# Optimization experiments

Hardware: AMD Instinct MI355X
Metric: run time of the kernel (lower is better)

The kernel has to match this reference:

```python
import jax, jax.numpy as jnp
import numpy as np

B, T, C, HS = 4, 2048, 2048, 64
H = C // HS
LW, LA, LV, LG = 64, 64, 32, 128
EPS_GN = 0.00064


def setup_inputs() -> dict:
    key = jax.random.key(0)
    ks = jax.random.split(key, 32)
    rn = lambda k, shape, s=1.0: jax.random.normal(k, shape, dtype=jnp.float32) * s
    return {
        "x": rn(ks[0], (B, T, C)),
        "v_first": rn(ks[1], (B, T, C)),
        "x_prev": rn(ks[2], (B, C)),
        "wkv_state": rn(ks[3], (B, H, HS, HS), 0.1),
        "x_r": rn(ks[4], (C,), 0.1),
        "x_w": rn(ks[5], (C,), 0.1),
        "x_k": rn(ks[6], (C,), 0.1),
        "x_v": rn(ks[7], (C,), 0.1),
        "x_a": rn(ks[8], (C,), 0.1),
        "x_g": rn(ks[9], (C,), 0.1),
        "w0": rn(ks[10], (C,), 0.1),
        "w1": rn(ks[11], (C, LW), 0.02),
        "w2": rn(ks[12], (LW, C), 0.02),
        "a0": rn(ks[13], (C,), 0.1),
        "a1": rn(ks[14], (C, LA), 0.02),
        "a2": rn(ks[15], (LA, C), 0.02),
        "v0": rn(ks[16], (C,), 0.1),
        "v1": rn(ks[17], (C, LV), 0.02),
        "v2": rn(ks[18], (LV, C), 0.02),
        "g1": rn(ks[19], (C, LG), 0.02),
        "g2": rn(ks[20], (LG, C), 0.02),
        "k_k": rn(ks[21], (C,), 0.1),
        "k_a": rn(ks[22], (C,), 0.1),
        "r_k": rn(ks[23], (H, HS), 0.1),
        "Wr": rn(ks[24], (C, C), 0.02),
        "Wk": rn(ks[25], (C, C), 0.02),
        "Wv": rn(ks[26], (C, C), 0.02),
        "Wo": rn(ks[27], (C, C), 0.02),
        "ln_w": jnp.ones((C,), dtype=jnp.float32),
        "ln_b": jnp.zeros((C,), dtype=jnp.float32),
    }


def _fwd(x, v_first, x_prev, wkv_state, x_r, x_w, x_k, x_v, x_a, x_g,
         w0, w1, w2, a0, a1, a2, v0, v1, v2, g1, g2, k_k, k_a, r_k,
         Wr, Wk, Wv, Wo, ln_w, ln_b):
    Bb, Tt, Cc = x.shape
    # token shift
    xx = jnp.concatenate([x_prev[:, None, :], x[:, :-1, :]], axis=1) - x
    xr = x + xx * x_r; xw = x + xx * x_w; xk = x + xx * x_k
    xv = x + xx * x_v; xa = x + xx * x_a; xg = x + xx * x_g
    r = xr @ Wr
    k = xk @ Wk
    v = xv @ Wv
    # log-decay: -softplus(-(w0 + tanh(xw@w1)@w2)) - 0.5  (<= -0.5)
    w_raw = -jax.nn.softplus(-(w0 + jnp.tanh(xw @ w1) @ w2)) - 0.5
    # layer_id != 0: mix with v_first
    v = v + (v_first - v) * jax.nn.sigmoid(v0 + (xv @ v1) @ v2)
    a = jax.nn.sigmoid(a0 + (xa @ a1) @ a2)
    g = jax.nn.sigmoid(xg @ g1) @ g2
    kk = (k * k_k).reshape(Bb, Tt, H, HS)
    kk = kk / jnp.maximum(jnp.linalg.norm(kk, axis=-1, keepdims=True), 1e-12)
    k = k * (1.0 + (a - 1.0) * k_a)
    rh = r.reshape(Bb, Tt, H, HS)
    kh = k.reshape(Bb, Tt, H, HS)
    vh = v.reshape(Bb, Tt, H, HS)
    ah = -kk                                  # removal direction
    bh = kk * a.reshape(Bb, Tt, H, HS)        # insertion direction
    wd = jnp.exp(-jnp.exp(w_raw)).reshape(Bb, Tt, H, HS)  # decay in (0,1)
    def step(st, ts):
        r_t, w_t, k_t, v_t, a_t, b_t = ts     # each [B,H,N]
        sa = jnp.einsum('bhij,bhj->bhi', st, a_t)
        st = st * w_t[:, :, None, :] + sa[..., None] * b_t[:, :, None, :] \
             + v_t[..., None] * k_t[:, :, None, :]
        return st, jnp.einsum('bhij,bhj->bhi', st, r_t)
    xs = tuple(jnp.moveaxis(t, 1, 0) for t in (rh, wd, kh, vh, ah, bh))
    _, out = jax.lax.scan(step, wkv_state, xs)
    out = jnp.moveaxis(out, 0, 1)             # [B,T,H,N]
    # GroupNorm(H groups) over each head's N channels
    mu = out.mean(-1, keepdims=True)
    var = out.var(-1, keepdims=True)
    out = ((out - mu) * jax.lax.rsqrt(var + EPS_GN)).reshape(Bb, Tt, Cc) * ln_w + ln_b
    bonus = (rh * kh * r_k).sum(-1, keepdims=True) * vh
    out = out + bonus.reshape(Bb, Tt, Cc)
    return (out * g) @ Wo


def reference(x, v_first, x_prev, wkv_state, x_r, x_w, x_k, x_v, x_a, x_g,
              w0, w1, w2, a0, a1, a2, v0, v1, v2, g1, g2, k_k, k_a, r_k,
              Wr, Wk, Wv, Wo, ln_w, ln_b):
    return _fwd(x, v_first, x_prev, wkv_state, x_r, x_w, x_k, x_v, x_a, x_g,
                w0, w1, w2, a0, a1, a2, v0, v1, v2, g1, g2, k_k, k_a, r_k,
                Wr, Wk, Wv, Wo, ln_w, ln_b)
```

## Files before the change

### kernel.cpp

```cpp
#include <hip/hip_runtime.h>

typedef float f32x4 __attribute__((ext_vector_type(4)));
typedef __bf16 bf16x8 __attribute__((ext_vector_type(8)));
typedef __bf16 bf16x4 __attribute__((ext_vector_type(4)));
typedef unsigned int u32x4 __attribute__((ext_vector_type(4)));

#define DI __device__ __forceinline__

constexpr int B_ = 4, T_ = 2048, C_ = 2048, H_ = 32;
constexpr int M_ = B_ * T_;

DI unsigned short f2bf(float f) {
  unsigned u = __float_as_uint(f);
  return (unsigned short)((u + 0x7FFFu + ((u >> 16) & 1u)) >> 16);
}
DI float bf2f(unsigned short h) { return __uint_as_float(((unsigned)h) << 16); }

DI void gl16(const void* g, void* l) {
  __builtin_amdgcn_global_load_lds(
      (__attribute__((address_space(1))) const unsigned int*)g,
      (__attribute__((address_space(3))) unsigned int*)l, 16, 0, 0);
}
DI void gl4(const void* g, void* l) {
  __builtin_amdgcn_global_load_lds(
      (__attribute__((address_space(1))) const unsigned int*)g,
      (__attribute__((address_space(3))) unsigned int*)l, 4, 0, 0);
}

DI float rsum16(float x) {
  int t = __builtin_amdgcn_update_dpp(0, __float_as_int(x), 0xB1, 0xF, 0xF, true);
  x += __int_as_float(t);
  t = __builtin_amdgcn_update_dpp(0, __float_as_int(x), 0x4E, 0xF, 0xF, true);
  x += __int_as_float(t);
  t = __builtin_amdgcn_update_dpp(0, __float_as_int(x), 0x124, 0xF, 0xF, true);
  x += __int_as_float(t);
  t = __builtin_amdgcn_update_dpp(0, __float_as_int(x), 0x128, 0xF, 0xF, true);
  x += __int_as_float(t);
  return x;
}

DI void tr_body(const float* __restrict__ in, unsigned short* __restrict__ out,
                int R, int C, int bx, int by, float (*tile)[33]) {
  int c0 = bx * 32, r0 = by * 32;
  int tx = threadIdx.x & 31, ty = threadIdx.x >> 5;
#pragma unroll
  for (int i = 0; i < 4; ++i) {
    int r = r0 + ty * 4 + i, c = c0 + tx;
    if (r < R && c < C) tile[ty * 4 + i][tx] = in[(size_t)r * C + c];
  }
  __syncthreads();
#pragma unroll
  for (int i = 0; i < 4; ++i) {
    int c = c0 + ty * 4 + i, r = r0 + tx;
    if (r < R && c < C) out[(size_t)c * R + r] = f2bf(tile[tx][ty * 4 + i]);
  }
}

__global__ __launch_bounds__(256) void k_transpose(const float* __restrict__ in,
                                                   unsigned short* __restrict__ out,
                                                   int R, int C) {
  __shared__ float tile[32][33];
  tr_body(in, out, R, C, blockIdx.x, blockIdx.y, tile);
}

__global__ __launch_bounds__(256) void k_transpose8(
    const float* w1, unsigned short* W1T, const float* a1, unsigned short* A1T,
    const float* v1, unsigned short* V1T, const float* g1, unsigned short* G1T,
    const float* w2, unsigned short* W2T, const float* a2, unsigned short* A2T,
    const float* v2, unsigned short* V2T, const float* g2, unsigned short* G2T) {
  __shared__ float tile[32][33];
  int b = blockIdx.x;
  if (b < 128)       tr_body(w1, W1T, 2048, 64, b % 2, b / 2, tile);
  else if (b < 256)  { b -= 128; tr_body(a1, A1T, 2048, 64, b % 2, b / 2, tile); }
  else if (b < 320)  { b -= 256; tr_body(v1, V1T, 2048, 32, 0, b, tile); }
  else if (b < 576)  { b -= 320; tr_body(g1, G1T, 2048, 128, b % 4, b / 4, tile); }
  else if (b < 704)  { b -= 576; tr_body(w2, W2T, 64, 2048, b % 64, b / 64, tile); }
  else if (b < 832)  { b -= 704; tr_body(a2, A2T, 64, 2048, b % 64, b / 64, tile); }
  else if (b < 896)  { b -= 832; tr_body(v2, V2T, 32, 2048, b % 64, b / 64, tile); }
  else               { b -= 896; tr_body(g2, G2T, 128, 2048, b % 64, b / 64, tile); }
}

DI void mix_emit(const float* coef, int c0, size_t off,
                 const float* xv, const float* dx, unsigned short* dst) {
  unsigned short u[8];
#pragma unroll
  for (int i = 0; i < 2; ++i) {
    f32x4 cf = *(const f32x4*)(coef + c0 + i * 4);
#pragma unroll
    for (int j = 0; j < 4; ++j) u[i * 4 + j] = f2bf(xv[i * 4 + j] + dx[i * 4 + j] * cf[j]);
  }
  u32x4 pv;
#pragma unroll
  for (int j = 0; j < 4; ++j) pv[j] = (unsigned)u[2 * j] | ((unsigned)u[2 * j + 1] << 16);
  *(u32x4*)(dst + off) = pv;
}

__global__ __launch_bounds__(256) void k_prep6(
    const float* __restrict__ x, const float* __restrict__ xprev,
    const float* __restrict__ cR, const float* __restrict__ cV,
    const float* __restrict__ cK, const float* __restrict__ cW,
    const float* __restrict__ cA, const float* __restrict__ cG,
    unsigned short* __restrict__ XR, unsigned short* __restrict__ XV,
    unsigned short* __restrict__ XK, unsigned short* __restrict__ XW,
    unsigned short* __restrict__ XA, unsigned short* __restrict__ XG) {
  int bt = blockIdx.x;
  int t = bt & (T_ - 1);
  int c0 = threadIdx.x * 8;
  size_t off = (size_t)bt * C_ + c0;
  const float* xp = x + off;
  const float* pp = t ? (xp - C_) : (xprev + (size_t)(bt >> 11) * C_ + c0);
  float xv[8], dx[8];
#pragma unroll
  for (int i = 0; i < 2; ++i) {
    f32x4 a = *(const f32x4*)(xp + i * 4);
    f32x4 p = *(const f32x4*)(pp + i * 4);
#pragma unroll
    for (int j = 0; j < 4; ++j) { xv[i * 4 + j] = a[j]; dx[i * 4 + j] = p[j] - a[j]; }
  }
  mix_emit(cR, c0, off, xv, dx, XR);
  mix_emit(cV, c0, off, xv, dx, XV);
  mix_emit(cK, c0, off, xv, dx, XK);
  mix_emit(cW, c0, off, xv, dx, XW);
  mix_emit(cA, c0, off, xv, dx, XA);
  mix_emit(cG, c0, off, xv, dx, XG);
}

template <int EPI>
__global__ __launch_bounds__(256, 2) void k_gemm_big(
    const unsigned short* __restrict__ A,
    const unsigned short* __restrict__ Bt,
    float* __restrict__ outF, unsigned short* __restrict__ outB,
    const unsigned short* __restrict__ svb, const float* __restrict__ vfirst,
    const unsigned short* __restrict__ abf,
    const float* __restrict__ k_k, const float* __restrict__ k_a,
    unsigned short* __restrict__ ahb, unsigned short* __restrict__ bhb) {
  __shared__ __align__(16) unsigned short As[128][64];
  __shared__ __align__(16) unsigned short Bs[128][64];
  const int tid = threadIdx.x, lane = tid & 63, wv = tid >> 6;
  const int bid = blockIdx.x;
  const int loc = bid >> 3;
  const int by = (bid & 7) * 8 + (loc & 7);
  const int bx = loc >> 3;
  const int m0 = by * 128, n0 = bx * 128;
  const int wm = (wv >> 1) * 64, wn = (wv & 1) * 64;
  const int lr = lane >> 3, lc = (lane & 7) * 8;
  f32x4 acc[4][4] = {};
  for (int kt = 0; kt < C_; kt += 64) {
    __syncthreads();
#pragma unroll
    for (int i = 0; i < 4; ++i) {
      int chunk = wv * 4 + i, r = chunk * 8 + lr;
      gl16(A + (size_t)(m0 + r) * C_ + kt + lc, (char*)&As[0][0] + chunk * 1024);
      gl16(Bt + (size_t)(n0 + r) * C_ + kt + lc, (char*)&Bs[0][0] + chunk * 1024);
    }
    __syncthreads();
    const int rr = lane & 15;
#pragma unroll
    for (int kh = 0; kh < 2; ++kh) {
      const int kof = kh * 32 + (lane >> 4) * 8;
      bf16x8 af[4], bfv[4];
#pragma unroll
      for (int i = 0; i < 4; ++i) af[i] = *(const bf16x8*)&As[wm + i * 16 + rr][kof];
#pragma unroll
      for (int j = 0; j < 4; ++j) bfv[j] = *(const bf16x8*)&Bs[wn + j * 16 + rr][kof];
#pragma unroll
      for (int i = 0; i < 4; ++i)
#pragma unroll
        for (int j = 0; j < 4; ++j)
          acc[i][j] = __builtin_amdgcn_mfma_f32_16x16x32_bf16(af[i], bfv[j], acc[i][j], 0, 0, 0);
    }
  }
  const int cr = (lane >> 4) * 4, cc2 = lane & 15;
  if constexpr (EPI == 2) {
    float kkv[4], kav[4];
#pragma unroll
    for (int j = 0; j < 4; ++j) {
      int col = n0 + wn + j * 16 + cc2;
      kkv[j] = k_k[col];
      kav[j] = k_a[col];
    }
#pragma unroll
    for (int i = 0; i < 4; ++i)
#pragma unroll
      for (int q = 0; q < 4; ++q) {
        int row = m0 + wm + i * 16 + cr + q;
        float kk4[4], p = 0.f;
#pragma unroll
        for (int j = 0; j < 4; ++j) {
          float kkc = acc[i][j][q] * kkv[j];
          kk4[j] = kkc;
          p += kkc * kkc;
        }
        p += __shfl_xor(p, 1); p += __shfl_xor(p, 2);
        p += __shfl_xor(p, 4); p += __shfl_xor(p, 8);
        float inv = 1.f / fmaxf(sqrtf(p), 1e-12f);
#pragma unroll
        for (int j = 0; j < 4; ++j) {
          int col = n0 + wn + j * 16 + cc2;
          size_t off = (size_t)row * C_ + col;
          float kkn = kk4[j] * inv;
          float a = bf2f(abf[off]);
          ahb[off] = f2bf(-kkn);
          bhb[off] = f2bf(kkn * a);
          outB[off] = f2bf(acc[i][j][q] * (1.f + (a - 1.f) * kav[j]));
        }
      }
  } else {
#pragma unroll
    for (int i = 0; i < 4; ++i)
#pragma unroll
      for (int j = 0; j < 4; ++j)
#pragma unroll
        for (int q = 0; q < 4; ++q) {
          int row = m0 + wm + i * 16 + cr + q;
          int col = n0 + wn + j * 16 + cc2;
          size_t off = (size_t)row * C_ + col;
          float v = acc[i][j][q];
          if constexpr (EPI == 0) {
            outB[off] = f2bf(v);
          } else if constexpr (EPI == 1) {
            float s = bf2f(svb[off]);
            outB[off] = f2bf(v + (vfirst[off] - v) * s);
          } else {
            outF[off] = v;
          }
        }
  }
}

template <int N, int ACT>
DI void down_body(int m0, unsigned short (*As)[64], unsigned short (*Bs)[64],
                  const unsigned short* __restrict__ A,
                  const unsigned short* __restrict__ Bt,
                  unsigned short* __restrict__ out) {
  const int tid = threadIdx.x, lane = tid & 63, wv = tid >> 6;
  const int wm = wv * 32;
  const int lr = lane >> 3, lc = (lane & 7) * 8;
  f32x4 acc[2][N / 16] = {};
  for (int kt = 0; kt < C_; kt += 64) {
    __syncthreads();
#pragma unroll
    for (int i = 0; i < 4; ++i) {
      int chunk = wv * 4 + i, r = chunk * 8 + lr;
      gl16(A + (size_t)(m0 + r) * C_ + kt + lc, (char*)&As[0][0] + chunk * 1024);
    }
#pragma unroll
    for (int i = 0; i < N / 32; ++i) {
      int chunk = wv * (N / 32) + i, r = chunk * 8 + lr;
      gl16(Bt + (size_t)r * C_ + kt + lc, (char*)&Bs[0][0] + chunk * 1024);
    }
    __syncthreads();
    const int rr = lane & 15;
#pragma unroll
    for (int kh = 0; kh < 2; ++kh) {
      const int kof = kh * 32 + (lane >> 4) * 8;
      bf16x8 af[2], bfv[N / 16];
#pragma unroll
      for (int i = 0; i < 2; ++i) af[i] = *(const bf16x8*)&As[wm + i * 16 + rr][kof];
#pragma unroll
      for (int j = 0; j < N / 16; ++j) bfv[j] = *(const bf16x8*)&Bs[j * 16 + rr][kof];
#pragma unroll
      for (int i = 0; i < 2; ++i)
#pragma unroll
        for (int j = 0; j < N / 16; ++j)
          acc[i][j] = __builtin_amdgcn_mfma_f32_16x16x32_bf16(af[i], bfv[j], acc[i][j], 0, 0, 0);
    }
  }
  const int cr = (lane >> 4) * 4, cc2 = lane & 15;
#pragma unroll
  for (int i = 0; i < 2; ++i)
#pragma unroll
    for (int j = 0; j < N / 16; ++j)
#pragma unroll
      for (int q = 0; q < 4; ++q) {
        int row = m0 + wm + i * 16 + cr + q;
        int col = j * 16 + cc2;
        float v = acc[i][j][q];
        if (ACT == 1) v = tanhf(v);
        else if (ACT == 2) v = 1.f / (1.f + expf(-v));
        out[(size_t)row * N + col] = f2bf(v);
      }
}

__global__ __launch_bounds__(256, 2) void k_down4(
    const unsigned short* __restrict__ XMw, const unsigned short* __restrict__ XMa,
    const unsigned short* __restrict__ XMv, const unsigned short* __restrict__ XMg,
    const unsigned short* __restrict__ W1T, const unsigned short* __restrict__ A1T,
    const unsigned short* __restrict__ V1T, const unsigned short* __restrict__ G1T,
    unsigned short* __restrict__ HWB, unsigned short* __restrict__ HAB,
    unsigned short* __restrict__ HVB, unsigned short* __restrict__ HGB) {
  __shared__ __align__(16) unsigned short As[128][64];
  __shared__ __align__(16) unsigned short Bs[128][64];
  int g = blockIdx.x >> 6;
  int m0 = (blockIdx.x & 63) * 128;
  if (g == 0)      down_body<64, 1>(m0, As, Bs, XMw, W1T, HWB);
  else if (g == 1) down_body<64, 0>(m0, As, Bs, XMa, A1T, HAB);
  else if (g == 2) down_body<32, 0>(m0, As, Bs, XMv, V1T, HVB);
  else             down_body<128, 2>(m0, As, Bs, XMg, G1T, HGB);
}

template <int K, int MODE>
__global__ __launch_bounds__(256, 2) void k_up(
    const unsigned short* __restrict__ A, const unsigned short* __restrict__ Bt,
    const float* __restrict__ bias, float* __restrict__ outF,
    unsigned short* __restrict__ outB) {
  __shared__ __align__(16) unsigned short As[128][K];
  __shared__ __align__(16) unsigned short Bs[128][K];
  const int tid = threadIdx.x, lane = tid & 63, wv = tid >> 6;
  const int m0 = blockIdx.y * 128, n0 = blockIdx.x * 128;
  const int wm = (wv >> 1) * 64, wn = (wv & 1) * 64;
  constexpr int LPR = K / 8;
  constexpr int RPC = 64 / LPR;
  const int lr = lane / LPR, lc = (lane % LPR) * 8;
  f32x4 acc[4][4] = {};
#pragma unroll
  for (int i = 0; i < K / 16; ++i) {
    int chunk = wv * (K / 16) + i;
    int r = chunk * RPC + lr;
    gl16(A + (size_t)(m0 + r) * K + lc, (char*)&As[0][0] + chunk * 1024);
    gl16(Bt + (size_t)(n0 + r) * K + lc, (char*)&Bs[0][0] + chunk * 1024);
  }
  __syncthreads();
  const int rr = lane & 15;
#pragma unroll
  for (int ks = 0; ks < K / 32; ++ks) {
    const int kof = ks * 32 + (lane >> 4) * 8;
    bf16x8 af[4], bfv[4];
#pragma unroll
    for (int i = 0; i < 4; ++i) af[i] = *(const bf16x8*)&As[wm + i * 16 + rr][kof];
#pragma unroll
    for (int j = 0; j < 4; ++j) bfv[j] = *(const bf16x8*)&Bs[wn + j * 16 + rr][kof];
#pragma unroll
    for (int i = 0; i < 4; ++i)
#pragma unroll
      for (int j = 0; j < 4; ++j)
        acc[i][j] = __builtin_amdgcn_mfma_f32_16x16x32_bf16(af[i], bfv[j], acc[i][j], 0, 0, 0);
  }
  const int cr = (lane >> 4) * 4, cc2 = lane & 15;
#pragma unroll
  for (int i = 0; i < 4; ++i)
#pragma unroll
    for (int j = 0; j < 4; ++j)
#pragma unroll
      for (int q = 0; q < 4; ++q) {
        int row = m0 + wm + i * 16 + cr + q;
        int col = n0 + wn + j * 16 + cc2;
        size_t off = (size_t)row * C_ + col;
        float up = acc[i][j][q];
        if (MODE == 0) {
          float z = -(bias[col] + up);
          float sp = fmaxf(z, 0.f) + log1pf(expf(-fabsf(z)));
          outF[off] = expf(-expf(-sp - 0.5f));
        } else if (MODE == 1) {
          outB[off] = f2bf(1.f / (1.f + expf(-(bias[col] + up))));
        } else {
          outB[off] = f2bf(up);
        }
      }
}

__global__ __launch_bounds__(64, 2) void k_scan(
    const unsigned short* __restrict__ RB, const float* __restrict__ WD,
    const unsigned short* __restrict__ KB, const unsigned short* __restrict__ VB,
    const unsigned short* __restrict__ AHB, const unsigned short* __restrict__ BHB,
    const float* __restrict__ s0, float* __restrict__ out) {
  __shared__ __align__(16) char sl[8][1024];
  const int lane = threadIdx.x & 63;
  const int p = blockIdx.x;
  const int wq = p >> 7, bh = p & 127;
  const int b = bh >> 5, h = bh & 31;
  const int e = lane & 15, rl = lane >> 4;
  const int row = wq * 4 + rl;
  const size_t base = (size_t)b * T_ * C_ + h * 64;
  f32x4 S = *(const f32x4*)(s0 + ((size_t)(b * H_ + h) * 64 + row) * 64 + e * 4);

  const char* srcA = (lane < 32 ? (const char*)RB : (const char*)KB) + (lane & 31) * 4;
  const char* srcB = (lane < 32 ? (const char*)AHB : (const char*)BHB) + (lane & 31) * 4;
  const char* srcW = (const char*)WD + lane * 4;
  const char* srcV = (const char*)VB + lane * 4;

  bf16x4 rv0, kv0, av0, bv0, rv1, kv1, av1, bv1;
  f32x4 wv0, wv1;
  unsigned short vi0, vi1;

#define ISSUE(t, slot)                                                        \
  {                                                                           \
    size_t ti = (size_t)((t) < T_ ? (t) : T_ - 1);                            \
    size_t eo = base + ti * C_;                                               \
    char* d = &sl[(slot)][0];                                                 \
    gl4(srcA + 2 * eo, d);                                                    \
    gl4(srcB + 2 * eo, d + 256);                                              \
    gl4(srcW + 4 * eo, d + 512);                                              \
    gl4(srcV + 2 * eo, d + 768);                                              \
  }

#define PREF(n, slot)                                                         \
  {                                                                           \
    const char* bp = &sl[(slot)][0];                                          \
    rv##n = *(const bf16x4*)(bp + e * 8);                                     \
    kv##n = *(const bf16x4*)(bp + 128 + e * 8);                               \
    av##n = *(const bf16x4*)(bp + 256 + e * 8);                               \
    bv##n = *(const bf16x4*)(bp + 384 + e * 8);                               \
    wv##n = *(const f32x4*)(bp + 512 + e * 16);                               \
    vi##n = *(const unsigned short*)(bp + 768 + row * 2);                     \
  }

#define COMPUTE(n, t)                                                         \
  {                                                                           \
    float rr[4], kk[4], aa[4], bb[4];                                         \
    _Pragma("unroll") for (int j = 0; j < 4; ++j) {                           \
      rr[j] = (float)rv##n[j];                                                \
      kk[j] = (float)kv##n[j];                                                \
      aa[j] = (float)av##n[j];                                                \
      bb[j] = (float)bv##n[j];                                                \
    }                                                                         \
    float sa = S[0] * aa[0];                                                  \
    sa = fmaf(S[1], aa[1], sa);                                               \
    sa = fmaf(S[2], aa[2], sa);                                               \
    sa = fmaf(S[3], aa[3], sa);                                               \
    sa = rsum16(sa);                                                          \
    float vi = bf2f(vi##n);                                                   \
    float o = 0.f;                                                            \
    _Pragma("unroll") for (int j = 0; j < 4; ++j) {                           \
      S[j] = fmaf(S[j], wv##n[j], fmaf(sa, bb[j], vi * kk[j]));               \
      o = fmaf(S[j], rr[j], o);                                               \
    }                                                                         \
    o = rsum16(o);                                                            \
    if (e == 0) out[base + (size_t)(t) * C_ + row] = o;                       \
  }

#define VMW asm volatile("s_waitcnt vmcnt(12)" ::: "memory")

  ISSUE(0, 0) ISSUE(1, 1) ISSUE(2, 2) ISSUE(3, 3)
  VMW;
  PREF(0, 0)
#pragma unroll 1
  for (int t = 0; t < T_; t += 8) {
    ISSUE(t + 4, 4)  VMW; PREF(1, 1) COMPUTE(0, t + 0)
    ISSUE(t + 5, 5)  VMW; PREF(0, 2) COMPUTE(1, t + 1)
    ISSUE(t + 6, 6)  VMW; PREF(1, 3) COMPUTE(0, t + 2)
    ISSUE(t + 7, 7)  VMW; PREF(0, 4) COMPUTE(1, t + 3)
    ISSUE(t + 8, 0)  VMW; PREF(1, 5) COMPUTE(0, t + 4)
    ISSUE(t + 9, 1)  VMW; PREF(0, 6) COMPUTE(1, t + 5)
    ISSUE(t + 10, 2) VMW; PREF(1, 7) COMPUTE(0, t + 6)
    ISSUE(t + 11, 3) VMW; PREF(0, 0) COMPUTE(1, t + 7)
  }
#undef ISSUE
#undef PREF
#undef COMPUTE
#undef VMW
}

__global__ __launch_bounds__(256) void k_gn(
    const float* __restrict__ o, const unsigned short* __restrict__ rb,
    const unsigned short* __restrict__ kb, const unsigned short* __restrict__ v,
    const unsigned short* __restrict__ g, const float* __restrict__ r_k,
    const float* __restrict__ lnw, const float* __restrict__ lnb,
    unsigned short* __restrict__ outg) {
  int wid = blockIdx.x * 4 + (threadIdx.x >> 6);
  int lane = threadIdx.x & 63;
  int h = wid & (H_ - 1);
  size_t bt = (size_t)(wid >> 5);
  size_t off = bt * C_ + h * 64 + lane;
  int c = h * 64 + lane;
  float x = o[off];
  float mu = x;
#pragma unroll
  for (int m = 1; m < 64; m <<= 1) mu += __shfl_xor(mu, m);
  mu *= (1.f / 64.f);
  float d = x - mu;
  float var = d * d;
#pragma unroll
  for (int m = 1; m < 64; m <<= 1) var += __shfl_xor(var, m);
  var *= (1.f / 64.f);
  float y = d * rsqrtf(var + 6.4e-4f) * lnw[c] + lnb[c];
  float bd = bf2f(rb[off]) * bf2f(kb[off]) * r_k[c];
#pragma unroll
  for (int m = 1; m < 64; m <<= 1) bd += __shfl_xor(bd, m);
  float res = (y + bd * bf2f(v[off])) * bf2f(g[off]);
  outg[off] = f2bf(res);
}

extern "C" void kernel_launch(void* const* d_in, const int* in_sizes, int n_in,
                              void* d_out, int out_size, void* d_ws, size_t ws_size,
                              hipStream_t stream) {
  const float* x      = (const float*)d_in[0];
  const float* vfirst = (const float*)d_in[1];
  const float* xprev  = (const float*)d_in[2];
  const float* wkv0   = (const float*)d_in[3];
  const float* x_r = (const float*)d_in[4];
  const float* x_w = (const float*)d_in[5];
  const float* x_k = (const float*)d_in[6];
  const float* x_v = (const float*)d_in[7];
  const float* x_a = (const float*)d_in[8];
  const float* x_g = (const float*)d_in[9];
  const float* w0 = (const float*)d_in[10];
  const float* w1 = (const float*)d_in[11];
  const float* w2 = (const float*)d_in[12];
  const float* a0 = (const float*)d_in[13];
  const float* a1 = (const float*)d_in[14];
  const float* a2 = (const float*)d_in[15];
  const float* v0 = (const float*)d_in[16];
  const float* v1 = (const float*)d_in[17];
  const float* v2 = (const float*)d_in[18];
  const float* g1 = (const float*)d_in[19];
  const float* g2 = (const float*)d_in[20];
  const float* k_k = (const float*)d_in[21];
  const float* k_a = (const float*)d_in[22];
  const float* r_k = (const float*)d_in[23];
  const float* Wr = (const float*)d_in[24];
  const float* Wk = (const float*)d_in[25];
  const float* Wv = (const float*)d_in[26];
  const float* Wo = (const float*)d_in[27];
  const float* lnw = (const float*)d_in[28];
  const float* lnb = (const float*)d_in[29];
  float* out = (float*)d_out;
  char* ws = (char*)d_ws;

  size_t woff = 0;
  auto alloc = [&](size_t n) { char* p = ws + woff; woff += n; return p; };
  char* R1 = alloc(67108864);
  unsigned short* ABF = (unsigned short*)R1;
  unsigned short* SVB = (unsigned short*)(R1 + 33554432);
  float* WD = (float*)R1;
  unsigned short* WT  = (unsigned short*)alloc(8388608);
  unsigned short* W1T = (unsigned short*)alloc(262144);
  unsigned short* A1T = (unsigned short*)alloc(262144);
  unsigned short* V1T = (unsigned short*)alloc(131072);
  unsigned short* G1T = (unsigned short*)alloc(524288);
  unsigned short* W2T = (unsigned short*)alloc(262144);
  unsigned short* A2T = (unsigned short*)alloc(262144);
  unsigned short* V2T = (unsigned short*)alloc(131072);
  unsigned short* G2T = (unsigned short*)alloc(524288);
  unsigned short* HWB = (unsigned short*)alloc(1048576);
  unsigned short* HAB = (unsigned short*)alloc(1048576);
  unsigned short* HVB = (unsigned short*)alloc(524288);
  unsigned short* HGB = (unsigned short*)alloc(2097152);
  unsigned short* RB  = (unsigned short*)alloc(33554432);
  unsigned short* KB  = (unsigned short*)alloc(33554432);
  unsigned short* VB  = (unsigned short*)alloc(33554432);
  unsigned short* AHB = (unsigned short*)alloc(33554432);
  unsigned short* BHB = (unsigned short*)alloc(33554432);
  alloc(65536);
  unsigned short* XMr = VB;
  unsigned short* XMv = KB;
  unsigned short* XMk = (unsigned short*)out;
  unsigned short* XMw = AHB;
  unsigned short* XMa = BHB;
  unsigned short* XMg = RB;
  unsigned short* GBF  = AHB;
  unsigned short* OUTG = BHB;

  dim3 blk(256);
  dim3 gg(16, 64);
  dim3 g1d(1024);

  k_transpose8<<<dim3(1152), blk, 0, stream>>>(w1, W1T, a1, A1T, v1, V1T, g1, G1T,
                                               w2, W2T, a2, A2T, v2, V2T, g2, G2T);

  k_prep6<<<dim3(M_), blk, 0, stream>>>(x, xprev, x_r, x_v, x_k, x_w, x_a, x_g,
                                        XMr, XMv, XMk, XMw, XMa, XMg);

  k_down4<<<dim3(256), blk, 0, stream>>>(XMw, XMa, XMv, XMg,
                                         W1T, A1T, V1T, G1T, HWB, HAB, HVB, HGB);

  k_up<64, 1><<<gg, blk, 0, stream>>>(HAB, A2T, a0, nullptr, ABF);
  k_up<32, 1><<<gg, blk, 0, stream>>>(HVB, V2T, v0, nullptr, SVB);

  k_transpose<<<dim3(64, 64), blk, 0, stream>>>(Wr, WT, 2048, 2048);
  k_gemm_big<0><<<g1d, blk, 0, stream>>>(XMr, WT,
      nullptr, RB, nullptr, nullptr, nullptr, nullptr, nullptr, nullptr, nullptr);

  k_transpose<<<dim3(64, 64), blk, 0, stream>>>(Wv, WT, 2048, 2048);
  k_gemm_big<1><<<g1d, blk, 0, stream>>>(XMv, WT,
      nullptr, VB, SVB, vfirst, nullptr, nullptr, nullptr, nullptr, nullptr);

  k_transpose<<<dim3(64, 64), blk, 0, stream>>>(Wk, WT, 2048, 2048);
  k_gemm_big<2><<<g1d, blk, 0, stream>>>(XMk, WT,
      nullptr, KB, nullptr, nullptr, ABF, k_k, k_a, AHB, BHB);

  k_up<64, 0><<<gg, blk, 0, stream>>>(HWB, W2T, w0, WD, nullptr);

  k_scan<<<dim3(2048), dim3(64), 0, stream>>>(RB, WD, KB, VB, AHB, BHB, wkv0, out);

  k_up<128, 3><<<gg, blk, 0, stream>>>(HGB, G2T, nullptr, nullptr, GBF);

  k_gn<<<dim3(65536), blk, 0, stream>>>(out, RB, KB, VB, GBF, r_k, lnw, lnb, OUTG);

  k_transpose<<<dim3(64, 64), blk, 0, stream>>>(Wo, WT, 2048, 2048);
  k_gemm_big<3><<<g1d, blk, 0, stream>>>(OUTG, WT,
      out, nullptr, nullptr, nullptr, nullptr, nullptr, nullptr, nullptr, nullptr);
}
```

Baseline: 1.284 ms.

## Split WKV scan state rows across more wavefronts with two elements per lane

The scan kernel now assigns 2 state rows per wavefront, with 32 lanes per row each holding 2 elements, instead of 4 rows with 16 lanes holding 4 elements. The grid doubles to 4096 blocks and launch bounds allow 4 blocks per SM. The aim is to shorten the serial per-step dependency chain and raise occupancy to hide latency. In exchange, each block loads the same per-timestep r/k/a/b/w/v data, so redundant global and LDS traffic doubles, and each reduction needs an extra cross-half shuffle.

```diff
diff --git a/kernel.cpp b/kernel.cpp
--- a/kernel.cpp
+++ b/kernel.cpp
@@ -1,8 +1,9 @@
 #include <hip/hip_runtime.h>
 
 typedef float f32x4 __attribute__((ext_vector_type(4)));
+typedef float f32x2 __attribute__((ext_vector_type(2)));
 typedef __bf16 bf16x8 __attribute__((ext_vector_type(8)));
-typedef __bf16 bf16x4 __attribute__((ext_vector_type(4)));
+typedef __bf16 bf16x2 __attribute__((ext_vector_type(2)));
 typedef unsigned int u32x4 __attribute__((ext_vector_type(4)));
 
 #define DI __device__ __forceinline__
@@ -359,7 +360,7 @@
       }
 }
 
-__global__ __launch_bounds__(64, 2) void k_scan(
+__global__ __launch_bounds__(64, 4) void k_scan(
     const unsigned short* __restrict__ RB, const float* __restrict__ WD,
     const unsigned short* __restrict__ KB, const unsigned short* __restrict__ VB,
     const unsigned short* __restrict__ AHB, const unsigned short* __restrict__ BHB,
@@ -369,18 +370,18 @@
   const int p = blockIdx.x;
   const int wq = p >> 7, bh = p & 127;
   const int b = bh >> 5, h = bh & 31;
-  const int e = lane & 15, rl = lane >> 4;
-  const int row = wq * 4 + rl;
+  const int e = lane & 31, rl = lane >> 5;
+  const int row = wq * 2 + rl;
   const size_t base = (size_t)b * T_ * C_ + h * 64;
-  f32x4 S = *(const f32x4*)(s0 + ((size_t)(b * H_ + h) * 64 + row) * 64 + e * 4);
+  f32x2 S = *(const f32x2*)(s0 + ((size_t)(b * H_ + h) * 64 + row) * 64 + e * 2);
 
   const char* srcA = (lane < 32 ? (const char*)RB : (const char*)KB) + (lane & 31) * 4;
   const char* srcB = (lane < 32 ? (const char*)AHB : (const char*)BHB) + (lane & 31) * 4;
   const char* srcW = (const char*)WD + lane * 4;
   const char* srcV = (const char*)VB + lane * 4;
 
-  bf16x4 rv0, kv0, av0, bv0, rv1, kv1, av1, bv1;
-  f32x4 wv0, wv1;
+  bf16x2 rv0, kv0, av0, bv0, rv1, kv1, av1, bv1;
+  f32x2 wv0, wv1;
   unsigned short vi0, vi1;
 
 #define ISSUE(t, slot)                                                        \
@@ -397,35 +398,29 @@
 #define PREF(n, slot)                                                         \
   {                                                                           \
     const char* bp = &sl[(slot)][0];                                          \
-    rv##n = *(const bf16x4*)(bp + e * 8);                                     \
-    kv##n = *(const bf16x4*)(bp + 128 + e * 8);                               \
-    av##n = *(const bf16x4*)(bp + 256 + e * 8);                               \
-    bv##n = *(const bf16x4*)(bp + 384 + e * 8);                               \
-    wv##n = *(const f32x4*)(bp + 512 + e * 16);                               \
+    rv##n = *(const bf16x2*)(bp + e * 4);                                     \
+    kv##n = *(const bf16x2*)(bp + 128 + e * 4);                               \
+    av##n = *(const bf16x2*)(bp + 256 + e * 4);                               \
+    bv##n = *(const bf16x2*)(bp + 384 + e * 4);                               \
+    wv##n = *(const f32x2*)(bp + 512 + e * 8);                                \
     vi##n = *(const unsigned short*)(bp + 768 + row * 2);                     \
   }
 
 #define COMPUTE(n, t)                                                         \
   {                                                                           \
-    float rr[4], kk[4], aa[4], bb[4];                                         \
-    _Pragma("unroll") for (int j = 0; j < 4; ++j) {                           \
-      rr[j] = (float)rv##n[j];                                                \
-      kk[j] = (float)kv##n[j];                                                \
-      aa[j] = (float)av##n[j];                                                \
-      bb[j] = (float)bv##n[j];                                                \
-    }                                                                         \
-    float sa = S[0] * aa[0];                                                  \
-    sa = fmaf(S[1], aa[1], sa);                                               \
-    sa = fmaf(S[2], aa[2], sa);                                               \
-    sa = fmaf(S[3], aa[3], sa);                                               \
+    float r0 = (float)rv##n[0], r1 = (float)rv##n[1];                         \
+    float k0 = (float)kv##n[0], k1 = (float)kv##n[1];                         \
+    float a0 = (float)av##n[0], a1 = (float)av##n[1];                         \
+    float b0 = (float)bv##n[0], b1 = (float)bv##n[1];                         \
+    float sa = fmaf(S[1], a1, S[0] * a0);                                     \
     sa = rsum16(sa);                                                          \
+    sa += __shfl_xor(sa, 16);                                                 \
     float vi = bf2f(vi##n);                                                   \
-    float o = 0.f;                                                            \
-    _Pragma("unroll") for (int j = 0; j < 4; ++j) {                           \
-      S[j] = fmaf(S[j], wv##n[j], fmaf(sa, bb[j], vi * kk[j]));               \
-      o = fmaf(S[j], rr[j], o);                                               \
-    }                                                                         \
+    S[0] = fmaf(S[0], wv##n[0], fmaf(sa, b0, vi * k0));                       \
+    S[1] = fmaf(S[1], wv##n[1], fmaf(sa, b1, vi * k1));                       \
+    float o = fmaf(S[1], r1, S[0] * r0);                                      \
     o = rsum16(o);                                                            \
+    o += __shfl_xor(o, 16);                                                   \
     if (e == 0) out[base + (size_t)(t) * C_ + row] = o;                       \
   }
 
@@ -581,7 +576,7 @@
 
   k_up<64, 0><<<gg, blk, 0, stream>>>(HWB, W2T, w0, WD, nullptr);
 
-  k_scan<<<dim3(2048), dim3(64), 0, stream>>>(RB, WD, KB, VB, AHB, BHB, wkv0, out);
+  k_scan<<<dim3(4096), dim3(64), 0, stream>>>(RB, WD, KB, VB, AHB, BHB, wkv0, out);
 
   k_up<128, 3><<<gg, blk, 0, stream>>>(HGB, G2T, nullptr, nullptr, GBF);
 
```

New measurement: 1.468 ms. +14.3%, slower.

## Double-buffer big GEMM LDS tiles with half-step prefetch pipeline

Applied to the files above, without the earlier changes.

Restructures the main bf16 GEMM K-loop from a load-barrier-compute-barrier pattern into a double-buffered pipeline. Each 64-wide K tile is split into two 32-wide halves, and the next halves are prefetched via global_load_lds while the current half is computed, with a partial vmcnt wait instead of a full drain. It also raises wave priority around the MFMA blocks. This is meant to hide global-to-LDS latency behind matrix math, at the cost of doubled LDS usage, which may reduce occupancy, and more fragile manual synchronization.

```diff
diff --git a/kernel.cpp b/kernel.cpp
--- a/kernel.cpp
+++ b/kernel.cpp
@@ -134,8 +134,8 @@
     const unsigned short* __restrict__ abf,
     const float* __restrict__ k_k, const float* __restrict__ k_a,
     unsigned short* __restrict__ ahb, unsigned short* __restrict__ bhb) {
-  __shared__ __align__(16) unsigned short As[128][64];
-  __shared__ __align__(16) unsigned short Bs[128][64];
+  __shared__ __align__(16) unsigned short Ab[2][2][128 * 32];
+  __shared__ __align__(16) unsigned short Bb[2][2][128 * 32];
   const int tid = threadIdx.x, lane = tid & 63, wv = tid >> 6;
   const int bid = blockIdx.x;
   const int loc = bid >> 3;
@@ -143,33 +143,65 @@
   const int bx = loc >> 3;
   const int m0 = by * 128, n0 = bx * 128;
   const int wm = (wv >> 1) * 64, wn = (wv & 1) * 64;
-  const int lr = lane >> 3, lc = (lane & 7) * 8;
+  const int srow = tid >> 2, scol = (tid & 3) * 8;
+  const unsigned short* Asrc = A + (size_t)(m0 + srow) * C_ + scol;
+  const unsigned short* Bsrc = Bt + (size_t)(n0 + srow) * C_ + scol;
+  const int rr = lane & 15;
+  const int kof = (lane >> 4) * 8;
+
+  auto stageA = [&](int bufi, int ks, int kt) {
+    char* d = (char*)&Ab[bufi][ks][0] + wv * 1024;
+    const unsigned short* s = Asrc + kt + ks * 32;
+    gl16(s, d);
+    gl16(s + (size_t)64 * C_, d + 4096);
+  };
+  auto stageB = [&](int bufi, int ks, int kt) {
+    char* d = (char*)&Bb[bufi][ks][0] + wv * 1024;
+    const unsigned short* s = Bsrc + kt + ks * 32;
+    gl16(s, d);
+    gl16(s + (size_t)64 * C_, d + 4096);
+  };
+
   f32x4 acc[4][4] = {};
-  for (int kt = 0; kt < C_; kt += 64) {
-    __syncthreads();
-#pragma unroll
-    for (int i = 0; i < 4; ++i) {
-      int chunk = wv * 4 + i, r = chunk * 8 + lr;
-      gl16(A + (size_t)(m0 + r) * C_ + kt + lc, (char*)&As[0][0] + chunk * 1024);
-      gl16(Bt + (size_t)(n0 + r) * C_ + kt + lc, (char*)&Bs[0][0] + chunk * 1024);
-    }
-    __syncthreads();
-    const int rr = lane & 15;
-#pragma unroll
-    for (int kh = 0; kh < 2; ++kh) {
-      const int kof = kh * 32 + (lane >> 4) * 8;
-      bf16x8 af[4], bfv[4];
-#pragma unroll
-      for (int i = 0; i < 4; ++i) af[i] = *(const bf16x8*)&As[wm + i * 16 + rr][kof];
-#pragma unroll
-      for (int j = 0; j < 4; ++j) bfv[j] = *(const bf16x8*)&Bs[wn + j * 16 + rr][kof];
-#pragma unroll
-      for (int i = 0; i < 4; ++i)
-#pragma unroll
-        for (int j = 0; j < 4; ++j)
-          acc[i][j] = __builtin_amdgcn_mfma_f32_16x16x32_bf16(af[i], bfv[j], acc[i][j], 0, 0, 0);
-    }
-  }
+
+  auto compute = [&](int bufi, int kh) {
+    bf16x8 af[4], bfv[4];
+#pragma unroll
+    for (int i = 0; i < 4; ++i)
+      af[i] = *(const bf16x8*)&Ab[bufi][kh][(wm + i * 16 + rr) * 32 + kof];
+#pragma unroll
+    for (int j2 = 0; j2 < 4; ++j2)
+      bfv[j2] = *(const bf16x8*)&Bb[bufi][kh][(wn + j2 * 16 + rr) * 32 + kof];
+    __builtin_amdgcn_s_setprio(1);
+#pragma unroll
+    for (int i = 0; i < 4; ++i)
+#pragma unroll
+      for (int j2 = 0; j2 < 4; ++j2)
+        acc[i][j2] = __builtin_amdgcn_mfma_f32_16x16x32_bf16(af[i], bfv[j2], acc[i][j2], 0, 0, 0);
+    __builtin_amdgcn_s_setprio(0);
+  };
+
+  stageA(0, 0, 0); stageB(0, 0, 0);
+  stageA(0, 1, 0); stageB(0, 1, 0);
+  stageA(1, 0, 64); stageB(1, 0, 64);
+  asm volatile("s_waitcnt vmcnt(4)" ::: "memory");
+  __builtin_amdgcn_s_barrier();
+
+#pragma unroll 1
+  for (int j = 0; j < 32; ++j) {
+    const int b = j & 1;
+    const int kt1 = (j + 1 < 32 ? j + 1 : 31) * 64;
+    const int kt2 = (j + 2 < 32 ? j + 2 : 31) * 64;
+    stageA(b ^ 1, 1, kt1); stageB(b ^ 1, 1, kt1);
+    compute(b, 0);
+    asm volatile("" ::: "memory");
+    __builtin_amdgcn_s_barrier();
+    stageA(b, 0, kt2); stageB(b, 0, kt2);
+    compute(b, 1);
+    asm volatile("s_waitcnt vmcnt(4)" ::: "memory");
+    __builtin_amdgcn_s_barrier();
+  }
+
   const int cr = (lane >> 4) * 4, cc2 = lane & 15;
   if constexpr (EPI == 2) {
     float kkv[4], kav[4];
```

Measured after the change: 1.351 ms. 5.2% more time.
